# Performance work log

Measured on AMD Instinct MI355X. Metric: run time of the kernel, lower is better.

Reference implementation:

```python
import jax, jax.numpy as jnp
import numpy as np


def setup_inputs() -> dict:
    key = jax.random.key(0)
    k1, k2, k3 = jax.random.split(key, 3)
    B, F, N = 8, 16, 2048
    # strictly positive features so momentum.log() is finite
    emb = jax.random.uniform(k1, (B, F, N), dtype=jnp.float32, minval=1e-3, maxval=1.0)
    # torch init: alpha * (rand(1,1)*0.02 + 0.99), beta * (rand(1,1,1)*0.02 + 0.99)
    alpha_p = 1.0 * (jax.random.uniform(k2, (1, 1), dtype=jnp.float32) * 0.02 + 0.99)
    beta_p = 1.0 * (jax.random.uniform(k3, (1, 1, 1), dtype=jnp.float32) * 0.02 + 0.99)
    return {"emb": emb, "alpha_p": alpha_p, "beta_p": beta_p}


def reference(emb, alpha_p, beta_p):
    # emb: [B, F, N]
    # pairwise squared distances over the feature dim:
    # sqdist[b,i,j] = ||e[:, i] - e[:, j]||^2 = n_i + n_j - 2 * <e_i, e_j>
    sq_norms = jnp.sum(emb * emb, axis=1)                 # [B, N]
    gram = jnp.einsum('bfi,bfj->bij', emb, emb)           # [B, N, N]
    sqdist = sq_norms[:, :, None] + sq_norms[:, None, :] - 2.0 * gram

    momentum = emb[:, 4, :]                               # [B, N]
    alpha = alpha_p[0, 0]                                 # scalar broadcast
    pow_momenta = jnp.exp(2.0 * alpha * jnp.log(momentum))  # momentum ** (2*alpha)
    # sym_min: min(p_i, p_j) pairwise -> [B, N, N]
    min_momenta = jnp.minimum(pow_momenta[:, :, None], pow_momenta[:, None, :])

    d_ij = sqdist * min_momenta                           # [B, N, N]
    # NOTE: _renorm in the source is computed then discarded (overwritten);
    # faithful math uses d_ij directly.
    beta_sq = beta_p[0, 0, 0] ** 2
    w_ij = jnp.exp(-beta_sq * d_ij)                       # [B, N, N]
    return w_ij
```

## Files before the change

### kernel.cpp

```cpp
#include <hip/hip_runtime.h>


#define BATCH 8
#define FDIM 16
#define NPT 2048
#define TI 32
#define TJ 1024
#define NTHREADS 512

__global__ __launch_bounds__(NTHREADS, 4) void qcd_aware_kernel(
    const float* __restrict__ emb,
    const float* __restrict__ alpha_p,
    const float* __restrict__ beta_p,
    float* __restrict__ out)
{
    __shared__ float Bs[FDIM][TJ];
    __shared__ float Af[FDIM][TI];
    __shared__ float nJ[TJ], qJ[TJ];
    __shared__ float nI[TI], qI[TI];

    const int b  = blockIdx.z;
    const int i0 = blockIdx.y * TI;
    const int j0 = blockIdx.x * TJ;
    const int t  = threadIdx.x;

    const float* base = emb + (size_t)b * FDIM * NPT;

    {
        float* BsF = &Bs[0][0];
        #pragma unroll
        for (int g = 0; g < 8; ++g) {
            const int w = 4 * t + 2048 * g;
            const int f = w >> 10;
            const int j = w & 1023;
            *(float4*)&BsF[w] = *(const float4*)(base + (size_t)f * NPT + j0 + j);
        }
        if (t < 128) {
            const int w = 4 * t;
            const int f = w >> 5;
            const int i = w & 31;
            *(float4*)(&Af[0][0] + w) = *(const float4*)(base + (size_t)f * NPT + i0 + i);
        }
    }
    __syncthreads();

    const float alpha2 = 2.0f * alpha_p[0];
    const float beta   = beta_p[0];
    const float qscale = -(beta * beta) * 1.4426950408889634f;

    {
        #pragma unroll
        for (int g = 0; g < 2; ++g) {
            const int c = t + NTHREADS * g;
            float s = 0.f;
            #pragma unroll
            for (int f = 0; f < FDIM; ++f) { float v = Bs[f][c]; s += v * v; }
            nJ[c] = s;
            qJ[c] = qscale * __expf(alpha2 * __logf(Bs[4][c]));
        }
        if (t < TI) {
            float s = 0.f;
            #pragma unroll
            for (int f = 0; f < FDIM; ++f) { float v = Af[f][t]; s += v * v; }
            nI[t] = s;
            qI[t] = qscale * __expf(alpha2 * __logf(Af[4][t]));
        }
    }
    __syncthreads();

    const int wv  = t >> 6;
    const int r0  = 4 * wv;
    const int tx4 = (t & 63) * 4;

    float acc[4][16] = {};
    #pragma unroll
    for (int f = 0; f < FDIM; ++f) {
        const float4 a = *(const float4*)&Af[f][r0];
        const float av[4] = {a.x, a.y, a.z, a.w};
        #pragma unroll
        for (int g = 0; g < 4; ++g) {
            const float4 bq = *(const float4*)&Bs[f][tx4 + 256 * g];
            const float bb[4] = {bq.x, bq.y, bq.z, bq.w};
            #pragma unroll
            for (int ii = 0; ii < 4; ++ii)
                #pragma unroll
                for (int jj = 0; jj < 4; ++jj)
                    acc[ii][g * 4 + jj] = fmaf(av[ii], bb[jj], acc[ii][g * 4 + jj]);
        }
    }

    #pragma unroll
    for (int g = 0; g < 4; ++g) {
        const float4 njv = *(const float4*)&nJ[tx4 + 256 * g];
        const float4 qjv = *(const float4*)&qJ[tx4 + 256 * g];
        const float nj[4] = {njv.x, njv.y, njv.z, njv.w};
        const float qj[4] = {qjv.x, qjv.y, qjv.z, qjv.w};
        #pragma unroll
        for (int ii = 0; ii < 4; ++ii) {
            const float ni = nI[r0 + ii];
            const float qi = qI[r0 + ii];
            float4 wo;
            float* wp = (float*)&wo;
            #pragma unroll
            for (int jj = 0; jj < 4; ++jj) {
                const float d = fmaf(-2.0f, acc[ii][g * 4 + jj], ni + nj[jj]);
                wp[jj] = __builtin_amdgcn_exp2f(fmaxf(qi, qj[jj]) * d);
            }
            const size_t rowp = ((size_t)b * NPT + (size_t)(i0 + r0 + ii)) * NPT + j0;
            *(float4*)(out + rowp + tx4 + 256 * g) = wo;
        }
    }
}

extern "C" void kernel_launch(void* const* d_in, const int* in_sizes, int n_in,
                              void* d_out, int out_size, void* d_ws, size_t ws_size,
                              hipStream_t stream) {
    const float* emb     = (const float*)d_in[0];
    const float* alpha_p = (const float*)d_in[1];
    const float* beta_p  = (const float*)d_in[2];
    float* out = (float*)d_out;

    dim3 grid(NPT / TJ, NPT / TI, BATCH);
    dim3 block(NTHREADS);
    qcd_aware_kernel<<<grid, block, 0, stream>>>(emb, alpha_p, beta_p, out);
}
```

Measured before the change: 148.5 us.

## Retile to 64x256 blocks with register-held B columns and inline column norms

Result: faster. 141.8 us (-4.5%).

```diff
diff --git a/kernel.cpp b/kernel.cpp
--- a/kernel.cpp
+++ b/kernel.cpp
@@ -4,42 +4,42 @@
 #define BATCH 8
 #define FDIM 16
 #define NPT 2048
-#define TI 32
-#define TJ 1024
-#define NTHREADS 512
+#define TI 64
+#define TJ 256
 
-__global__ __launch_bounds__(NTHREADS, 4) void qcd_aware_kernel(
+__global__ __launch_bounds__(256, 4) void qcd_aware_kernel(
     const float* __restrict__ emb,
     const float* __restrict__ alpha_p,
     const float* __restrict__ beta_p,
     float* __restrict__ out)
 {
+    __shared__ float As[FDIM][TI];
     __shared__ float Bs[FDIM][TJ];
-    __shared__ float Af[FDIM][TI];
-    __shared__ float nJ[TJ], qJ[TJ];
     __shared__ float nI[TI], qI[TI];
 
     const int b  = blockIdx.z;
     const int i0 = blockIdx.y * TI;
     const int j0 = blockIdx.x * TJ;
-    const int t  = threadIdx.x;
+    const int t    = threadIdx.x;
+    const int lane = t & 63;
+    const int wv   = t >> 6;
 
     const float* base = emb + (size_t)b * FDIM * NPT;
 
     {
         float* BsF = &Bs[0][0];
         #pragma unroll
-        for (int g = 0; g < 8; ++g) {
-            const int w = 4 * t + 2048 * g;
-            const int f = w >> 10;
-            const int j = w & 1023;
-            *(float4*)&BsF[w] = *(const float4*)(base + (size_t)f * NPT + j0 + j);
+        for (int g = 0; g < 4; ++g) {
+            const int wd = 4 * t + 1024 * g;
+            const int f  = wd >> 8;
+            const int j  = wd & 255;
+            *(float4*)&BsF[wd] = *(const float4*)(base + (size_t)f * NPT + j0 + j);
         }
-        if (t < 128) {
-            const int w = 4 * t;
-            const int f = w >> 5;
-            const int i = w & 31;
-            *(float4*)(&Af[0][0] + w) = *(const float4*)(base + (size_t)f * NPT + i0 + i);
+        {
+            const int wd = 4 * t;
+            const int f  = wd >> 6;
+            const int i  = wd & 63;
+            *(float4*)(&As[0][0] + wd) = *(const float4*)(base + (size_t)f * NPT + i0 + i);
         }
     }
     __syncthreads();
@@ -48,66 +48,80 @@
     const float beta   = beta_p[0];
     const float qscale = -(beta * beta) * 1.4426950408889634f;
 
-    {
+    if (t < TI) {
+        float s = 0.f;
         #pragma unroll
-        for (int g = 0; g < 2; ++g) {
-            const int c = t + NTHREADS * g;
-            float s = 0.f;
-            #pragma unroll
-            for (int f = 0; f < FDIM; ++f) { float v = Bs[f][c]; s += v * v; }
-            nJ[c] = s;
-            qJ[c] = qscale * __expf(alpha2 * __logf(Bs[4][c]));
-        }
-        if (t < TI) {
-            float s = 0.f;
-            #pragma unroll
-            for (int f = 0; f < FDIM; ++f) { float v = Af[f][t]; s += v * v; }
-            nI[t] = s;
-            qI[t] = qscale * __expf(alpha2 * __logf(Af[4][t]));
-        }
+        for (int f = 0; f < FDIM; ++f) { const float v = As[f][t]; s += v * v; }
+        nI[t] = s;
+        qI[t] = qscale * __expf(alpha2 * __logf(As[4][t]));
     }
     __syncthreads();
 
-    const int wv  = t >> 6;
-    const int r0  = 4 * wv;
-    const int tx4 = (t & 63) * 4;
+    const int c4    = lane * 4;
+    const int rbase = wv * 16;
 
-    float acc[4][16] = {};
+    float bc[FDIM][4];
+    float nj[4] = {0.f, 0.f, 0.f, 0.f};
+    float qj[4];
+
+    float acc0[4][4] = {};
     #pragma unroll
     for (int f = 0; f < FDIM; ++f) {
-        const float4 a = *(const float4*)&Af[f][r0];
+        const float4 bq = *(const float4*)&Bs[f][c4];
+        bc[f][0] = bq.x; bc[f][1] = bq.y; bc[f][2] = bq.z; bc[f][3] = bq.w;
+        #pragma unroll
+        for (int jj = 0; jj < 4; ++jj) nj[jj] = fmaf(bc[f][jj], bc[f][jj], nj[jj]);
+        const float4 a = *(const float4*)&As[f][rbase];
         const float av[4] = {a.x, a.y, a.z, a.w};
         #pragma unroll
-        for (int g = 0; g < 4; ++g) {
-            const float4 bq = *(const float4*)&Bs[f][tx4 + 256 * g];
-            const float bb[4] = {bq.x, bq.y, bq.z, bq.w};
+        for (int ii = 0; ii < 4; ++ii)
+            #pragma unroll
+            for (int jj = 0; jj < 4; ++jj)
+                acc0[ii][jj] = fmaf(av[ii], bc[f][jj], acc0[ii][jj]);
+    }
+    #pragma unroll
+    for (int jj = 0; jj < 4; ++jj)
+        qj[jj] = qscale * __expf(alpha2 * __logf(bc[4][jj]));
+
+    #pragma unroll
+    for (int r = 0; r < 4; ++r) {
+        const int row = rbase + r;
+        const float ni = nI[row];
+        const float qi = qI[row];
+        float4 wo; float* wp = (float*)&wo;
+        #pragma unroll
+        for (int jj = 0; jj < 4; ++jj) {
+            const float d = fmaf(-2.0f, acc0[r][jj], ni + nj[jj]);
+            wp[jj] = __builtin_amdgcn_exp2f(fmaxf(qi, qj[jj]) * d);
+        }
+        *(float4*)(out + ((size_t)b * NPT + (size_t)(i0 + row)) * NPT + j0 + c4) = wo;
+    }
+
+    #pragma unroll
+    for (int p = 1; p < 4; ++p) {
+        float acc[4][4] = {};
+        #pragma unroll
+        for (int f = 0; f < FDIM; ++f) {
+            const float4 a = *(const float4*)&As[f][rbase + 4 * p];
+            const float av[4] = {a.x, a.y, a.z, a.w};
             #pragma unroll
             for (int ii = 0; ii < 4; ++ii)
                 #pragma unroll
                 for (int jj = 0; jj < 4; ++jj)
-                    acc[ii][g * 4 + jj] = fmaf(av[ii], bb[jj], acc[ii][g * 4 + jj]);
+                    acc[ii][jj] = fmaf(av[ii], bc[f][jj], acc[ii][jj]);
         }
-    }
-
-    #pragma unroll
-    for (int g = 0; g < 4; ++g) {
-        const float4 njv = *(const float4*)&nJ[tx4 + 256 * g];
-        const float4 qjv = *(const float4*)&qJ[tx4 + 256 * g];
-        const float nj[4] = {njv.x, njv.y, njv.z, njv.w};
-        const float qj[4] = {qjv.x, qjv.y, qjv.z, qjv.w};
         #pragma unroll
-        for (int ii = 0; ii < 4; ++ii) {
-            const float ni = nI[r0 + ii];
-            const float qi = qI[r0 + ii];
-            float4 wo;
-            float* wp = (float*)&wo;
+        for (int r = 0; r < 4; ++r) {
+            const int row = rbase + 4 * p + r;
+            const float ni = nI[row];
+            const float qi = qI[row];
+            float4 wo; float* wp = (float*)&wo;
             #pragma unroll
             for (int jj = 0; jj < 4; ++jj) {
-                const float d = fmaf(-2.0f, acc[ii][g * 4 + jj], ni + nj[jj]);
+                const float d = fmaf(-2.0f, acc[r][jj], ni + nj[jj]);
                 wp[jj] = __builtin_amdgcn_exp2f(fmaxf(qi, qj[jj]) * d);
             }
-            const size_t rowp = ((size_t)b * NPT + (size_t)(i0 + r0 + ii)) * NPT + j0;
-            *(float4*)(out + rowp + tx4 + 256 * g) = wo;
+            *(float4*)(out + ((size_t)b * NPT + (size_t)(i0 + row)) * NPT + j0 + c4) = wo;
         }
     }
 }
@@ -121,6 +135,6 @@
     float* out = (float*)d_out;
 
     dim3 grid(NPT / TJ, NPT / TI, BATCH);
-    dim3 block(NTHREADS);
+    dim3 block(256);
     qcd_aware_kernel<<<grid, block, 0, stream>>>(emb, alpha_p, beta_p, out);
 }
```
